# Optimization experiments

Hardware: AMD Instinct MI355X
Metric: run time of the kernel (lower is better)

## Reference

```python
import jax, jax.numpy as jnp
import numpy as np

B, T, D = 16, 2048, 256

def setup_inputs() -> dict:
    key = jax.random.key(0)
    k1, k2, k3 = jax.random.split(key, 3)
    q = jax.random.normal(k1, (B, T, D), dtype=jnp.float32)
    a = jax.random.normal(k2, (B, T, D), dtype=jnp.float32)
    # original uses 'uniform' init; scale ~ small
    U = jax.random.uniform(k3, (D, D), dtype=jnp.float32, minval=-0.05, maxval=0.05)
    return {"q": q, "a": a, "U": U}

def reference(q, a, U):
    # G[b,i,j] = tanh( (q[b,i,:] @ U) . a[b,j,:] )
    qU = jnp.einsum('btd,de->bte', q, U)                 # [B,Tq,D]
    G = jnp.tanh(jnp.einsum('btd,bsd->bts', qU, a))      # [B,Tq,Ta]
    g_q = jax.nn.softmax(jnp.max(G, axis=-1), axis=1)    # [B,Tq]
    g_a = jax.nn.softmax(jnp.max(G, axis=1), axis=1)     # [B,Ta]
    q_out = jnp.einsum('btd,bt->bd', q, g_q)             # [B,D]
    a_out = jnp.einsum('bsd,bs->bd', a, g_a)             # [B,D]
    return (q_out, a_out)
```

## Files before the change

### kernel.cpp

```cpp
#include <hip/hip_runtime.h>
#include <stdint.h>

typedef __attribute__((ext_vector_type(8))) short s8v;
typedef __attribute__((ext_vector_type(4))) float f4v;

__device__ __forceinline__ unsigned short f2bf(float f) {
  unsigned u = __float_as_uint(f);
  u = u + 0x7FFFu + ((u >> 16) & 1u);
  return (unsigned short)(u >> 16);
}
__device__ __forceinline__ float bf2f(unsigned short h) {
  return __uint_as_float((unsigned)h << 16);
}
__device__ __forceinline__ unsigned encf(float f) {
  unsigned i = __float_as_uint(f);
  return (i & 0x80000000u) ? ~i : (i | 0x80000000u);
}
__device__ __forceinline__ float decf(unsigned u) {
  unsigned i = (u & 0x80000000u) ? (u & 0x7FFFFFFFu) : ~u;
  return __uint_as_float(i);
}
__device__ __forceinline__ void gload_lds16(const unsigned short* g, unsigned short* l) {
  __builtin_amdgcn_global_load_lds((const __attribute__((address_space(1))) void*)g,
                                   (__attribute__((address_space(3))) void*)l, 16, 0, 0);
}

__global__ void convert_kernel(const float4* __restrict__ q, const float4* __restrict__ a,
                               const float* __restrict__ U,
                               ushort4* __restrict__ qb, ushort4* __restrict__ ab,
                               unsigned short* __restrict__ Ut) {
  const int bx = blockIdx.x;
  if (bx < 8192) {
    const int i = bx * 256 + threadIdx.x;
    float4 v = q[i];
    qb[i] = make_ushort4(f2bf(v.x), f2bf(v.y), f2bf(v.z), f2bf(v.w));
    float4 w = a[i];
    ab[i] = make_ushort4(f2bf(w.x), f2bf(w.y), f2bf(w.z), f2bf(w.w));
  } else {
    const int idx = (bx - 8192) * 256 + threadIdx.x;
    const int n  = idx >> 6;
    const int k4 = (idx & 63) * 4;
    ushort4 o;
    o.x = f2bf(U[(k4 + 0) * 256 + n]);
    o.y = f2bf(U[(k4 + 1) * 256 + n]);
    o.z = f2bf(U[(k4 + 2) * 256 + n]);
    o.w = f2bf(U[(k4 + 3) * 256 + n]);
    *(ushort4*)&Ut[n * 256 + k4] = o;
  }
}

template<int WM, int WN, int MODE>
__global__ void gemm_bt(const unsigned short* __restrict__ A,
                        const unsigned short* __restrict__ Bm,
                        long strideA, long strideB,
                        unsigned short* __restrict__ C,
                        unsigned* __restrict__ rowmax,
                        unsigned* __restrict__ colmax) {
  constexpr int T = WM * WN * 64;
  constexpr int AROWS = WM * 64;
  constexpr int BROWS = WN * 64;
  constexpr int RPI = T / 8;

  __shared__ unsigned short As[AROWS * 64];
  __shared__ unsigned short Bs[BROWS * 64];
  __shared__ unsigned rowLds[AROWS];
  __shared__ unsigned colLds[BROWS];

  const int tid = threadIdx.x;
  int tm, tn, b;
  if (MODE == 1) { b = blockIdx.x; tn = blockIdx.y; tm = blockIdx.z; }
  else           { tm = blockIdx.x; tn = blockIdx.y; b = blockIdx.z; }
  const unsigned short* Ab = A + (long)b * strideA + (long)tm * AROWS * 256;
  const unsigned short* Bb = Bm + (long)b * strideB + (long)tn * BROWS * 256;

  const int lane = tid & 63;
  const int m16  = lane & 15;
  const int quad = lane >> 4;
  const int wave = tid >> 6;
  const int wm   = wave / WN, wn = wave % WN;
  const int srow = tid >> 3;
  const int scol = (((tid & 7) ^ (srow & 7))) * 8;

  if (MODE == 1) {
    if (tid < AROWS) rowLds[tid] = 0u;
    if (tid < BROWS) colLds[tid] = 0u;
  }

  f4v acc[4][4] = {};

  for (int kt = 0; kt < 4; ++kt) {
    const int k0 = kt * 64;
    __syncthreads();
    #pragma unroll
    for (int i = 0; i < AROWS / RPI; ++i) {
      const int r = i * RPI + srow;
      gload_lds16(Ab + (long)r * 256 + k0 + scol, &As[i * RPI * 64 + tid * 8]);
    }
    #pragma unroll
    for (int i = 0; i < BROWS / RPI; ++i) {
      const int r = i * RPI + srow;
      gload_lds16(Bb + (long)r * 256 + k0 + scol, &Bs[i * RPI * 64 + tid * 8]);
    }
    __syncthreads();
    #pragma unroll
    for (int kk = 0; kk < 2; ++kk) {
      const int cs = ((kk * 4 + quad) ^ (m16 & 7)) * 8;
      s8v af[4], bfv[4];
      #pragma unroll
      for (int i = 0; i < 4; ++i)
        af[i] = *(const s8v*)&As[(wm * 64 + i * 16 + m16) * 64 + cs];
      #pragma unroll
      for (int j = 0; j < 4; ++j)
        bfv[j] = *(const s8v*)&Bs[(wn * 64 + j * 16 + m16) * 64 + cs];
      #pragma unroll
      for (int i = 0; i < 4; ++i)
        #pragma unroll
        for (int j = 0; j < 4; ++j)
          acc[i][j] = __builtin_amdgcn_mfma_f32_16x16x32_bf16(af[i], bfv[j], acc[i][j], 0, 0, 0);
    }
  }

  if (MODE == 0) {
    #pragma unroll
    for (int i = 0; i < 4; ++i)
      #pragma unroll
      for (int r = 0; r < 4; ++r) {
        const long row = (long)tm * AROWS + wm * 64 + i * 16 + quad * 4 + r;
        #pragma unroll
        for (int j = 0; j < 4; ++j) {
          const int col = tn * BROWS + wn * 64 + j * 16 + m16;
          C[row * 256 + col] = f2bf(acc[i][j][r]);
        }
      }
  } else {
    #pragma unroll
    for (int i = 0; i < 4; ++i)
      #pragma unroll
      for (int r = 0; r < 4; ++r) {
        float v = fmaxf(fmaxf(acc[i][0][r], acc[i][1][r]), fmaxf(acc[i][2][r], acc[i][3][r]));
        #pragma unroll
        for (int d2 = 1; d2 < 16; d2 <<= 1) v = fmaxf(v, __shfl_xor(v, d2));
        if (m16 == 0) atomicMax(&rowLds[wm * 64 + i * 16 + quad * 4 + r], encf(v));
      }
    #pragma unroll
    for (int j = 0; j < 4; ++j) {
      float v = -3.4e38f;
      #pragma unroll
      for (int i = 0; i < 4; ++i)
        #pragma unroll
        for (int r = 0; r < 4; ++r) v = fmaxf(v, acc[i][j][r]);
      v = fmaxf(v, __shfl_xor(v, 16));
      v = fmaxf(v, __shfl_xor(v, 32));
      if (quad == 0) atomicMax(&colLds[wn * 64 + j * 16 + m16], encf(v));
    }
    __syncthreads();
    if (tid < AROWS) {
      atomicMax(&rowmax[(long)b * 2048 + tm * AROWS + tid], rowLds[tid]);
    } else if (tid < AROWS + BROWS) {
      atomicMax(&colmax[(long)b * 2048 + tn * BROWS + (tid - AROWS)], colLds[tid - AROWS]);
    }
  }
}

__global__ void wsum_kernel(const ushort4* __restrict__ qb, const ushort4* __restrict__ ab,
                            const unsigned* __restrict__ rowmax, const unsigned* __restrict__ colmax,
                            float* __restrict__ out) {
  const int tid = threadIdx.x;
  const int chunk = blockIdx.x;
  const int b = blockIdx.y;
  const int z = blockIdx.z;
  const unsigned* e = z ? colmax : rowmax;
  const ushort4* src = z ? ab : qb;

  __shared__ float sm[4];
  __shared__ float ss[4];
  __shared__ float wLds[128];
  __shared__ float red[256 * 4];

  float x[8];
  float m = -3.4e38f;
  #pragma unroll
  for (int j = 0; j < 8; ++j) {
    x[j] = tanhf(decf(e[b * 2048 + j * 256 + tid]));
    m = fmaxf(m, x[j]);
  }
  #pragma unroll
  for (int d2 = 1; d2 < 64; d2 <<= 1) m = fmaxf(m, __shfl_xor(m, d2));
  if ((tid & 63) == 0) sm[tid >> 6] = m;
  __syncthreads();
  m = fmaxf(fmaxf(sm[0], sm[1]), fmaxf(sm[2], sm[3]));
  float s = 0.f;
  #pragma unroll
  for (int j = 0; j < 8; ++j) s += expf(x[j] - m);
  #pragma unroll
  for (int d2 = 1; d2 < 64; d2 <<= 1) s += __shfl_xor(s, d2);
  if ((tid & 63) == 0) ss[tid >> 6] = s;
  __syncthreads();
  const float inv = 1.f / (ss[0] + ss[1] + ss[2] + ss[3]);

  if (tid < 128) {
    float xv = tanhf(decf(e[b * 2048 + chunk * 128 + tid]));
    wLds[tid] = expf(xv - m) * inv;
  }
  __syncthreads();

  const int dg = tid & 63;
  const int rg = tid >> 6;
  float a0 = 0.f, a1 = 0.f, a2 = 0.f, a3 = 0.f;
  const long rowbase = (long)b * 2048 + chunk * 128;
  for (int t = rg; t < 128; t += 4) {
    const float w = wLds[t];
    ushort4 v = src[(rowbase + t) * 64 + dg];
    a0 += w * bf2f(v.x); a1 += w * bf2f(v.y);
    a2 += w * bf2f(v.z); a3 += w * bf2f(v.w);
  }
  red[tid * 4 + 0] = a0; red[tid * 4 + 1] = a1;
  red[tid * 4 + 2] = a2; red[tid * 4 + 3] = a3;
  __syncthreads();
  if (tid < 64) {
    #pragma unroll
    for (int k = 0; k < 4; ++k) {
      float v = red[(0 * 64 + tid) * 4 + k] + red[(1 * 64 + tid) * 4 + k] +
                red[(2 * 64 + tid) * 4 + k] + red[(3 * 64 + tid) * 4 + k];
      atomicAdd(&out[z * 4096 + b * 256 + tid * 4 + k], v);
    }
  }
}

extern "C" void kernel_launch(void* const* d_in, const int* in_sizes, int n_in,
                              void* d_out, int out_size, void* d_ws, size_t ws_size,
                              hipStream_t stream) {
  const float* q = (const float*)d_in[0];
  const float* a = (const float*)d_in[1];
  const float* U = (const float*)d_in[2];
  float* out = (float*)d_out;

  char* w = (char*)d_ws;
  unsigned short* qb = (unsigned short*)w;
  unsigned short* ab = (unsigned short*)(w + (16ull << 20));
  unsigned short* qU = (unsigned short*)(w + (32ull << 20));
  unsigned short* Ut = (unsigned short*)(w + (48ull << 20));
  unsigned* rmax = (unsigned*)(w + (48ull << 20) + (128ull << 10));
  unsigned* cmax = rmax + 32768;

  hipMemsetAsync(rmax, 0, 2 * 32768 * sizeof(unsigned), stream);
  hipMemsetAsync(out, 0, 8192 * sizeof(float), stream);

  convert_kernel<<<8192 + 64, 256, 0, stream>>>((const float4*)q, (const float4*)a, U,
                                                (ushort4*)qb, (ushort4*)ab, Ut);

  gemm_bt<2, 2, 0><<<dim3(256, 2, 1), 256, 0, stream>>>(qb, Ut, 0, 0, qU, nullptr, nullptr);

  gemm_bt<2, 2, 1><<<dim3(16, 16, 16), 256, 0, stream>>>(qU, ab, 2048 * 256, 2048 * 256,
                                                         nullptr, rmax, cmax);

  wsum_kernel<<<dim3(16, 16, 2), 256, 0, stream>>>((const ushort4*)qb, (const ushort4*)ab,
                                                   rmax, cmax, out);
}
```

Measured before the change: 181.5 us.

## Widen GEMM N-tile for the score pass and fold memsets into kernels

The GEMM template is reparameterized so the attention-score pass uses a 128x256 block tile, with each wave holding 4x8 MFMA accumulators, where it previously used 128x128. The qU GEMM keeps a 128x128 tile. The two hipMemsetAsync calls are removed: the rowmax/colmax buffers are zeroed by extra blocks in the convert kernel, and the output is zeroed inside the score GEMM. The wider tile halves the grid and reloads of the A tile, and more accumulators per wave raise register pressure. Zeroing the output inside the GEMM relies on kernel ordering within the stream.

```diff
diff --git a/kernel.cpp b/kernel.cpp
--- a/kernel.cpp
+++ b/kernel.cpp
@@ -28,7 +28,8 @@
 __global__ void convert_kernel(const float4* __restrict__ q, const float4* __restrict__ a,
                                const float* __restrict__ U,
                                ushort4* __restrict__ qb, ushort4* __restrict__ ab,
-                               unsigned short* __restrict__ Ut) {
+                               unsigned short* __restrict__ Ut,
+                               unsigned* __restrict__ rcmax) {
   const int bx = blockIdx.x;
   if (bx < 8192) {
     const int i = bx * 256 + threadIdx.x;
@@ -36,7 +37,7 @@
     qb[i] = make_ushort4(f2bf(v.x), f2bf(v.y), f2bf(v.z), f2bf(v.w));
     float4 w = a[i];
     ab[i] = make_ushort4(f2bf(w.x), f2bf(w.y), f2bf(w.z), f2bf(w.w));
-  } else {
+  } else if (bx < 8256) {
     const int idx = (bx - 8192) * 256 + threadIdx.x;
     const int n  = idx >> 6;
     const int k4 = (idx & 63) * 4;
@@ -46,20 +47,23 @@
     o.z = f2bf(U[(k4 + 2) * 256 + n]);
     o.w = f2bf(U[(k4 + 3) * 256 + n]);
     *(ushort4*)&Ut[n * 256 + k4] = o;
-  }
-}
-
-template<int WM, int WN, int MODE>
+  } else {
+    const int idx = (bx - 8256) * 256 + threadIdx.x;
+    *(uint4*)&rcmax[idx * 4] = make_uint4(0u, 0u, 0u, 0u);
+  }
+}
+
+template<int WNT, int MODE>
 __global__ void gemm_bt(const unsigned short* __restrict__ A,
                         const unsigned short* __restrict__ Bm,
                         long strideA, long strideB,
                         unsigned short* __restrict__ C,
                         unsigned* __restrict__ rowmax,
-                        unsigned* __restrict__ colmax) {
-  constexpr int T = WM * WN * 64;
-  constexpr int AROWS = WM * 64;
-  constexpr int BROWS = WN * 64;
-  constexpr int RPI = T / 8;
+                        unsigned* __restrict__ colmax,
+                        float* __restrict__ outz) {
+  constexpr int AROWS = 128;
+  constexpr int BROWS = 32 * WNT;
+  constexpr int RPI = 32;
 
   __shared__ unsigned short As[AROWS * 64];
   __shared__ unsigned short Bs[BROWS * 64];
@@ -77,16 +81,20 @@
   const int m16  = lane & 15;
   const int quad = lane >> 4;
   const int wave = tid >> 6;
-  const int wm   = wave / WN, wn = wave % WN;
+  const int wm   = wave >> 1, wn = wave & 1;
   const int srow = tid >> 3;
   const int scol = (((tid & 7) ^ (srow & 7))) * 8;
 
   if (MODE == 1) {
     if (tid < AROWS) rowLds[tid] = 0u;
     if (tid < BROWS) colLds[tid] = 0u;
-  }
-
-  f4v acc[4][4] = {};
+    if (tn == 0 && tm == 0) {
+      outz[b * 256 + tid] = 0.f;
+      outz[4096 + b * 256 + tid] = 0.f;
+    }
+  }
+
+  f4v acc[4][WNT] = {};
 
   for (int kt = 0; kt < 4; ++kt) {
     const int k0 = kt * 64;
@@ -105,18 +113,17 @@
     #pragma unroll
     for (int kk = 0; kk < 2; ++kk) {
       const int cs = ((kk * 4 + quad) ^ (m16 & 7)) * 8;
-      s8v af[4], bfv[4];
+      s8v af[4];
       #pragma unroll
       for (int i = 0; i < 4; ++i)
         af[i] = *(const s8v*)&As[(wm * 64 + i * 16 + m16) * 64 + cs];
       #pragma unroll
-      for (int j = 0; j < 4; ++j)
-        bfv[j] = *(const s8v*)&Bs[(wn * 64 + j * 16 + m16) * 64 + cs];
-      #pragma unroll
-      for (int i = 0; i < 4; ++i)
-        #pragma unroll
-        for (int j = 0; j < 4; ++j)
-          acc[i][j] = __builtin_amdgcn_mfma_f32_16x16x32_bf16(af[i], bfv[j], acc[i][j], 0, 0, 0);
+      for (int j = 0; j < WNT; ++j) {
+        s8v bf = *(const s8v*)&Bs[(wn * (16 * WNT) + j * 16 + m16) * 64 + cs];
+        #pragma unroll
+        for (int i = 0; i < 4; ++i)
+          acc[i][j] = __builtin_amdgcn_mfma_f32_16x16x32_bf16(af[i], bf, acc[i][j], 0, 0, 0);
+      }
     }
   }
 
@@ -127,8 +134,8 @@
       for (int r = 0; r < 4; ++r) {
         const long row = (long)tm * AROWS + wm * 64 + i * 16 + quad * 4 + r;
         #pragma unroll
-        for (int j = 0; j < 4; ++j) {
-          const int col = tn * BROWS + wn * 64 + j * 16 + m16;
+        for (int j = 0; j < WNT; ++j) {
+          const int col = tn * BROWS + wn * (16 * WNT) + j * 16 + m16;
           C[row * 256 + col] = f2bf(acc[i][j][r]);
         }
       }
@@ -137,13 +144,15 @@
     for (int i = 0; i < 4; ++i)
       #pragma unroll
       for (int r = 0; r < 4; ++r) {
-        float v = fmaxf(fmaxf(acc[i][0][r], acc[i][1][r]), fmaxf(acc[i][2][r], acc[i][3][r]));
+        float v = -3.4e38f;
+        #pragma unroll
+        for (int j = 0; j < WNT; ++j) v = fmaxf(v, acc[i][j][r]);
         #pragma unroll
         for (int d2 = 1; d2 < 16; d2 <<= 1) v = fmaxf(v, __shfl_xor(v, d2));
         if (m16 == 0) atomicMax(&rowLds[wm * 64 + i * 16 + quad * 4 + r], encf(v));
       }
     #pragma unroll
-    for (int j = 0; j < 4; ++j) {
+    for (int j = 0; j < WNT; ++j) {
       float v = -3.4e38f;
       #pragma unroll
       for (int i = 0; i < 4; ++i)
@@ -151,14 +160,13 @@
         for (int r = 0; r < 4; ++r) v = fmaxf(v, acc[i][j][r]);
       v = fmaxf(v, __shfl_xor(v, 16));
       v = fmaxf(v, __shfl_xor(v, 32));
-      if (quad == 0) atomicMax(&colLds[wn * 64 + j * 16 + m16], encf(v));
+      if (quad == 0) atomicMax(&colLds[wn * (16 * WNT) + j * 16 + m16], encf(v));
     }
     __syncthreads();
-    if (tid < AROWS) {
+    if (tid < AROWS)
       atomicMax(&rowmax[(long)b * 2048 + tm * AROWS + tid], rowLds[tid]);
-    } else if (tid < AROWS + BROWS) {
-      atomicMax(&colmax[(long)b * 2048 + tn * BROWS + (tid - AROWS)], colLds[tid - AROWS]);
-    }
+    if (tid < BROWS)
+      atomicMax(&colmax[(long)b * 2048 + tn * BROWS + tid], colLds[tid]);
   }
 }
 
@@ -243,16 +251,14 @@
   unsigned* rmax = (unsigned*)(w + (48ull << 20) + (128ull << 10));
   unsigned* cmax = rmax + 32768;
 
-  hipMemsetAsync(rmax, 0, 2 * 32768 * sizeof(unsigned), stream);
-  hipMemsetAsync(out, 0, 8192 * sizeof(float), stream);
-
-  convert_kernel<<<8192 + 64, 256, 0, stream>>>((const float4*)q, (const float4*)a, U,
-                                                (ushort4*)qb, (ushort4*)ab, Ut);
-
-  gemm_bt<2, 2, 0><<<dim3(256, 2, 1), 256, 0, stream>>>(qb, Ut, 0, 0, qU, nullptr, nullptr);
-
-  gemm_bt<2, 2, 1><<<dim3(16, 16, 16), 256, 0, stream>>>(qU, ab, 2048 * 256, 2048 * 256,
-                                                         nullptr, rmax, cmax);
+  convert_kernel<<<8192 + 64 + 64, 256, 0, stream>>>((const float4*)q, (const float4*)a, U,
+                                                     (ushort4*)qb, (ushort4*)ab, Ut, rmax);
+
+  gemm_bt<4, 0><<<dim3(256, 2, 1), 256, 0, stream>>>(qb, Ut, 0, 0, qU,
+                                                     nullptr, nullptr, nullptr);
+
+  gemm_bt<8, 1><<<dim3(16, 8, 16), 256, 0, stream>>>(qU, ab, 2048 * 256, 2048 * 256,
+                                                     nullptr, rmax, cmax, out);
 
   wsum_kernel<<<dim3(16, 16, 2), 256, 0, stream>>>((const ushort4*)qb, (const ushort4*)ab,
                                                    rmax, cmax, out);
```

Result: slower. 430.4 us (+137.1%).
